# Kernel optimization log

Hardware: AMD Instinct MI355X
Metric: run time of the kernel (lower is better)

The kernel has to match this reference:

```python
import jax, jax.numpy as jnp
import numpy as np

C = 256          # channels
NUM_HEADS = 4
HEAD_DIM = C // NUM_HEADS
TILE_SIZE = 64
TILE_SEQ = TILE_SIZE * TILE_SIZE  # 4096
B, H_IMG, W_IMG = 1, 96, 96
EPS = 1e-5


def setup_inputs() -> dict:
    key = jax.random.key(0)
    k0, k1, k2 = jax.random.split(key, 3)
    x = jax.random.normal(k0, (B, C, H_IMG, W_IMG), jnp.float32)
    norm_w = jnp.ones((C,), jnp.float32)
    norm_b = jnp.zeros((C,), jnp.float32)
    qkv_w = jax.random.normal(k1, (3 * C, C), jnp.float32) * (C ** -0.5)
    qkv_b = jnp.zeros((3 * C,), jnp.float32)
    proj_w = jax.random.normal(k2, (C, C), jnp.float32) * (C ** -0.5)
    proj_b = jnp.zeros((C,), jnp.float32)
    return {"x": x, "norm_w": norm_w, "norm_b": norm_b,
            "qkv_w": qkv_w, "qkv_b": qkv_b,
            "proj_w": proj_w, "proj_b": proj_b}


def _attn(q, k, v, scale):
    # q: [B,H,Q,D], k/v: [B,H,K,D]
    s = jnp.einsum('bhqd,bhkd->bhqk', q, k) * scale
    p = jax.nn.softmax(s, axis=-1)
    return jnp.einsum('bhqk,bhkd->bhqd', p, v)


def reference(x, norm_w, norm_b, qkv_w, qkv_b, proj_w, proj_b):
    b, c, h, w = x.shape
    seq = h * w
    g = min(32, c)
    # GroupNorm
    xg = x.reshape(b, g, c // g, h, w)
    mean = xg.mean(axis=(2, 3, 4), keepdims=True)
    var = ((xg - mean) ** 2).mean(axis=(2, 3, 4), keepdims=True)
    xn = (xg - mean) * jax.lax.rsqrt(var + EPS)
    xn = xn.reshape(b, c, h, w) * norm_w[None, :, None, None] + norm_b[None, :, None, None]
    # flatten spatial -> tokens
    xf = xn.transpose(0, 2, 3, 1).reshape(b, seq, c)
    qkv = xf @ qkv_w.T + qkv_b  # [B,S,3C]
    qkv = qkv.reshape(b, seq, 3, NUM_HEADS, HEAD_DIM).transpose(2, 0, 3, 1, 4)
    q, k, v = qkv[0], qkv[1], qkv[2]  # [B,H,S,D]
    scale = HEAD_DIM ** -0.5
    if seq > TILE_SEQ:
        num_tiles = (seq + TILE_SEQ - 1) // TILE_SEQ
        outs = []
        for i in range(num_tiles):  # small fixed tile count, static slices
            s0 = i * TILE_SEQ
            e0 = min((i + 1) * TILE_SEQ, seq)
            k0 = max(0, s0 - TILE_SEQ // 2)
            k1 = min(seq, e0 + TILE_SEQ // 2)
            outs.append(_attn(q[:, :, s0:e0], k[:, :, k0:k1], v[:, :, k0:k1], scale))
        out = jnp.concatenate(outs, axis=2)
    else:
        out = _attn(q, k, v, scale)
    out = out.transpose(0, 2, 1, 3).reshape(b, seq, c)
    out = out @ proj_w.T + proj_b
    out = out.reshape(b, h, w, c).transpose(0, 3, 1, 2)
    return out + x
```

## Files before the change

### kernel.cpp

```cpp
#include <hip/hip_runtime.h>

typedef __bf16 bf16x8 __attribute__((ext_vector_type(8)));
typedef float f32x4 __attribute__((ext_vector_type(4)));
typedef float f32x16 __attribute__((ext_vector_type(16)));
typedef int i32x4 __attribute__((ext_vector_type(4)));
typedef int i32x2 __attribute__((ext_vector_type(2)));
typedef unsigned short u16x4 __attribute__((ext_vector_type(4)));

#define S_TOK 9216
#define LOG2E 1.44269504088896340736f
#define SCALE_Q (0.125f * LOG2E)

__device__ inline unsigned short f2bf(float f) {
    unsigned int u = __builtin_bit_cast(unsigned int, f);
    return (unsigned short)((u + 0x7fffu + ((u >> 16) & 1u)) >> 16);
}

__device__ inline unsigned int cvt_pk_bf16(float lo, float hi) {
    unsigned int r;
    asm("v_cvt_pk_bf16_f32 %0, %1, %2" : "=v"(r) : "v"(lo), "v"(hi));
    return r;
}

__device__ inline void permswap(unsigned int& a, unsigned int& b) {
    asm("v_permlane32_swap_b32 %0, %1" : "+v"(a), "+v"(b));
}

__device__ inline f32x4 MFMA(bf16x8 a, bf16x8 b, f32x4 c) {
    return __builtin_amdgcn_mfma_f32_16x16x32_bf16(a, b, c, 0, 0, 0);
}
__device__ inline f32x16 MFMA32(bf16x8 a, bf16x8 b, f32x16 c) {
    return __builtin_amdgcn_mfma_f32_32x32x16_bf16(a, b, c, 0, 0, 0);
}

__device__ inline int swz(int row, int c) {
    return ((c + (row >> 3)) & 7) ^ (row & 7);
}
__device__ inline bf16x8 load_frag(const unsigned short* lds, int outer, int kbase) {
    int lane = threadIdx.x & 63;
    int row = outer + (lane & 15);
    int cc = swz(row, (kbase >> 3) + (lane >> 4));
    return *reinterpret_cast<const bf16x8*>(lds + row * 64 + cc * 8);
}
__device__ inline bf16x8 load_frag32(const unsigned short* lds, int outer, int kbase) {
    int lane = threadIdx.x & 63;
    int row = outer + (lane & 31);
    int cc = swz(row, (kbase >> 3) + (lane >> 5));
    return *reinterpret_cast<const bf16x8*>(lds + row * 64 + cc * 8);
}
__device__ inline void stage_tile(unsigned short* lds, const unsigned short* src,
                                  int stride, int nrows) {
    for (int id = threadIdx.x; id < nrows * 8; id += 256) {
        int row = id >> 3, cc = id & 7;
        i32x4 v = *reinterpret_cast<const i32x4*>(src + row * stride + cc * 8);
        *reinterpret_cast<i32x4*>(lds + row * 64 + swz(row, cc) * 8) = v;
    }
}

__global__ __launch_bounds__(256) void gn_stats_part(const float* __restrict__ x,
                                                     float* __restrict__ part) {
    int c = blockIdx.x;
    const f32x4* p = reinterpret_cast<const f32x4*>(x + c * S_TOK);
    float s = 0.f, ss = 0.f;
    for (int i = threadIdx.x; i < 2304; i += 256) {
        f32x4 v = p[i];
        s += v[0] + v[1] + v[2] + v[3];
        ss += v[0] * v[0] + v[1] * v[1] + v[2] * v[2] + v[3] * v[3];
    }
#pragma unroll
    for (int off = 1; off < 64; off <<= 1) {
        s += __shfl_xor(s, off);
        ss += __shfl_xor(ss, off);
    }
    __shared__ float rs[4], rss[4];
    int wave = threadIdx.x >> 6;
    if ((threadIdx.x & 63) == 0) { rs[wave] = s; rss[wave] = ss; }
    __syncthreads();
    if (threadIdx.x == 0) {
        part[c] = rs[0] + rs[1] + rs[2] + rs[3];
        part[256 + c] = rss[0] + rss[1] + rss[2] + rss[3];
    }
}

__global__ __launch_bounds__(256) void gn_apply(const float* __restrict__ x,
                                                const float* __restrict__ part,
                                                const float* __restrict__ nw,
                                                const float* __restrict__ nb,
                                                unsigned short* __restrict__ xf) {
    __shared__ float tl[64][65];
    __shared__ float gmean[8], grstd[8];
    int sb = blockIdx.x * 64, cb = blockIdx.y * 64;
    if (threadIdx.x < 8) {
        int g = (cb >> 3) + threadIdx.x;
        float s = 0.f, ss = 0.f;
#pragma unroll
        for (int i = 0; i < 8; ++i) { s += part[g * 8 + i]; ss += part[256 + g * 8 + i]; }
        float mean = s * (1.f / 73728.f);
        float var = ss * (1.f / 73728.f) - mean * mean;
        gmean[threadIdx.x] = mean;
        grstd[threadIdx.x] = rsqrtf(var + 1e-5f);
    }
    __syncthreads();
    for (int id = threadIdx.x; id < 1024; id += 256) {
        int cr = id >> 4;
        int sq = (id & 15) << 2;
        int c = cb + cr;
        f32x4 v = *reinterpret_cast<const f32x4*>(x + c * S_TOK + sb + sq);
        float mu = gmean[cr >> 3], rstd = grstd[cr >> 3];
        float wv = nw[c] * rstd;
        float bv = nb[c] - mu * wv;
#pragma unroll
        for (int j = 0; j < 4; ++j) tl[sq + j][cr] = v[j] * wv + bv;
    }
    __syncthreads();
    for (int id = threadIdx.x; id < 1024; id += 256) {
        int sr = id >> 4;
        int cq = (id & 15) << 2;
        u16x4 o;
#pragma unroll
        for (int j = 0; j < 4; ++j) o[j] = f2bf(tl[sr][cq + j]);
        *reinterpret_cast<u16x4*>(xf + (sb + sr) * 256 + cb + cq) = o;
    }
}

__global__ __launch_bounds__(256) void conv_both(const float* __restrict__ qkvw_in,
                                                 const float* __restrict__ projw_in,
                                                 unsigned short* __restrict__ out) {
    int i = blockIdx.x * 256 + threadIdx.x;
    float v;
    if (i < 768 * 256) v = qkvw_in[i] * ((i < 256 * 256) ? SCALE_Q : 1.0f);
    else v = projw_in[i - 768 * 256];
    out[i] = f2bf(v);
}

template <int MODE>
__global__ __launch_bounds__(256) void gemm_bt(const unsigned short* __restrict__ A,
                                               const unsigned short* __restrict__ B,
                                               const float* __restrict__ bias,
                                               unsigned short* __restrict__ q_out,
                                               unsigned short* __restrict__ k_out,
                                               unsigned short* __restrict__ vT_out,
                                               const float* __restrict__ xres,
                                               float* __restrict__ out) {
    __shared__ alignas(16) unsigned short As[128 * 64];
    __shared__ alignas(16) unsigned short Bs[128 * 64];
    int mb = blockIdx.x, nb = blockIdx.y;
    int wave = threadIdx.x >> 6, lane = threadIdx.x & 63;
    int wm = wave >> 1, wn = wave & 1;
    f32x4 zero = {0.f, 0.f, 0.f, 0.f};
    f32x4 acc[4][4];
    for (int i = 0; i < 4; ++i)
        for (int j = 0; j < 4; ++j) acc[i][j] = zero;
    for (int ks = 0; ks < 4; ++ks) {
        __syncthreads();
        stage_tile(As, A + (mb * 128) * 256 + ks * 64, 256, 128);
        stage_tile(Bs, B + (nb * 128) * 256 + ks * 64, 256, 128);
        __syncthreads();
#pragma unroll
        for (int kk = 0; kk < 2; ++kk) {
            bf16x8 af[4], bfr[4];
#pragma unroll
            for (int mt = 0; mt < 4; ++mt) af[mt] = load_frag(As, wm * 64 + mt * 16, kk * 32);
#pragma unroll
            for (int nt = 0; nt < 4; ++nt) bfr[nt] = load_frag(Bs, wn * 64 + nt * 16, kk * 32);
#pragma unroll
            for (int mt = 0; mt < 4; ++mt)
#pragma unroll
                for (int nt = 0; nt < 4; ++nt)
                    acc[mt][nt] = MFMA(af[mt], bfr[nt], acc[mt][nt]);
        }
    }
    int r0 = (lane >> 4) << 2;
    int cl = lane & 15;
#pragma unroll
    for (int mt = 0; mt < 4; ++mt) {
#pragma unroll
        for (int nt = 0; nt < 4; ++nt) {
            int m = mb * 128 + wm * 64 + mt * 16 + r0;
            int n = nb * 128 + wn * 64 + nt * 16 + cl;
            if (MODE == 0) {
                float bv = bias[n] * ((n < 256) ? SCALE_Q : 1.0f);
                if (n < 256) {
#pragma unroll
                    for (int r = 0; r < 4; ++r)
                        q_out[(m + r) * 256 + n] = f2bf(acc[mt][nt][r] + bv);
                } else if (n < 512) {
#pragma unroll
                    for (int r = 0; r < 4; ++r)
                        k_out[(m + r) * 256 + (n - 256)] = f2bf(acc[mt][nt][r] + bv);
                } else {
                    u16x4 o;
#pragma unroll
                    for (int r = 0; r < 4; ++r) o[r] = f2bf(acc[mt][nt][r] + bv);
                    *reinterpret_cast<u16x4*>(vT_out + (n - 512) * S_TOK + m) = o;
                }
            } else {
                float bv = bias[n];
                f32x4 xr = *reinterpret_cast<const f32x4*>(xres + n * S_TOK + m);
                f32x4 o;
#pragma unroll
                for (int r = 0; r < 4; ++r) o[r] = acc[mt][nt][r] + bv + xr[r];
                *reinterpret_cast<f32x4*>(out + n * S_TOK + m) = o;
            }
        }
    }
}

struct StageRegs { i32x4 k0, k1, v0, v1; };

__device__ inline StageRegs load_stage(const unsigned short* ksrc, const unsigned short* vsrc) {
    int tid = threadIdx.x;
    int row = tid >> 3, cc = tid & 7;
    StageRegs r;
    r.k0 = *reinterpret_cast<const i32x4*>(ksrc + row * 256 + cc * 8);
    r.k1 = *reinterpret_cast<const i32x4*>(ksrc + (row + 32) * 256 + cc * 8);
    r.v0 = *reinterpret_cast<const i32x4*>(vsrc + row * S_TOK + cc * 8);
    r.v1 = *reinterpret_cast<const i32x4*>(vsrc + (row + 32) * S_TOK + cc * 8);
    return r;
}

__device__ inline void store_stage(unsigned short* K, unsigned short* V, StageRegs r) {
    int tid = threadIdx.x;
    int row = tid >> 3, cc = tid & 7;
    *reinterpret_cast<i32x4*>(K + row * 64 + swz(row, cc) * 8) = r.k0;
    *reinterpret_cast<i32x4*>(K + (row + 32) * 64 + swz(row + 32, cc) * 8) = r.k1;
    *reinterpret_cast<i32x4*>(V + row * 64 + swz(row, cc) * 8) = r.v0;
    *reinterpret_cast<i32x4*>(V + (row + 32) * 64 + swz(row + 32, cc) * 8) = r.v1;
}

__device__ inline bf16x8 mkpa(const f32x16& sc, int b, float& lrun) {
    float E0 = __builtin_amdgcn_exp2f(sc[b + 0]);
    float E1 = __builtin_amdgcn_exp2f(sc[b + 1]);
    float E2 = __builtin_amdgcn_exp2f(sc[b + 2]);
    float E3 = __builtin_amdgcn_exp2f(sc[b + 3]);
    float E4 = __builtin_amdgcn_exp2f(sc[b + 4]);
    float E5 = __builtin_amdgcn_exp2f(sc[b + 5]);
    float E6 = __builtin_amdgcn_exp2f(sc[b + 6]);
    float E7 = __builtin_amdgcn_exp2f(sc[b + 7]);
    lrun += ((E0 + E1) + (E2 + E3)) + ((E4 + E5) + (E6 + E7));
    unsigned int w0 = cvt_pk_bf16(E0, E1);
    unsigned int w1 = cvt_pk_bf16(E2, E3);
    unsigned int w2 = cvt_pk_bf16(E4, E5);
    unsigned int w3 = cvt_pk_bf16(E6, E7);
    permswap(w0, w2);
    permswap(w1, w3);
    i32x4 w;
    w[0] = (int)w0; w[1] = (int)w1; w[2] = (int)w2; w[3] = (int)w3;
    return __builtin_bit_cast(bf16x8, w);
}

template <int NC>
__global__ __launch_bounds__(256) void attn(const unsigned short* __restrict__ qb,
                                            const unsigned short* __restrict__ kb,
                                            const unsigned short* __restrict__ vT,
                                            unsigned short* __restrict__ Opart,
                                            float* __restrict__ lpart) {
    __shared__ alignas(16) unsigned short LDS[4 * 4096];
    unsigned short* Ks0 = LDS;
    unsigned short* Ks1 = LDS + 4096;
    unsigned short* Vs0 = LDS + 8192;
    unsigned short* Vs1 = LDS + 12288;
    constexpr int NS0 = 96 / NC, NS1 = 112 / NC, NS2 = 48 / NC;
    constexpr int B0 = 16 * NS0, B1 = B0 + 16 * NS1, NB = B1 + 4 * NS2;
    static_assert(NC % 2 == 0 && NC >= 4, "NC even");

    int bx = blockIdx.x;
    int head = bx / NB;
    int r = bx % NB;
    int tile, seg, qi;
    if (r < B0)      { tile = 0; seg = r >> 4; qi = r & 15; }
    else if (r < B1) { int t = r - B0; tile = 1; seg = t >> 4; qi = t & 15; }
    else             { int t = r - B1; tile = 2; seg = t >> 2; qi = t & 3; }
    int qs0 = (tile == 0) ? 0 : (tile == 1 ? 4096 : 8192);
    int kv0 = (tile == 0) ? 0 : (tile == 1 ? 2048 : 6144);
    int qstart = qs0 + qi * 256;
    int c0 = seg * NC;
    int wave = threadIdx.x >> 6, lane = threadIdx.x & 63;
    int l31 = lane & 31, h = lane >> 5;

    stage_tile(LDS, qb + qstart * 256 + head * 64, 256, 256);
    __syncthreads();
    bf16x8 qfA[4], qfB[4];
#pragma unroll
    for (int s = 0; s < 4; ++s) {
        qfA[s] = load_frag32(LDS, wave * 64, s * 16);
        qfB[s] = load_frag32(LDS, wave * 64 + 32, s * 16);
    }
    __syncthreads();

    f32x16 oA0, oA1, oB0, oB1;
#pragma unroll
    for (int i = 0; i < 16; ++i) { oA0[i] = 0.f; oA1[i] = 0.f; oB0[i] = 0.f; oB1[i] = 0.f; }
    float lA = 0.f, lB = 0.f;

    const unsigned short* kbase = kb + kv0 * 256 + head * 64;
    const unsigned short* vbase = vT + head * 64 * S_TOK + kv0;

    auto compute = [&](const unsigned short* Kp, const unsigned short* Vp) {
        __builtin_amdgcn_s_setprio(1);
#pragma unroll
        for (int half = 0; half < 2; ++half) {
            f32x16 sc0, sc1;
#pragma unroll
            for (int i = 0; i < 16; ++i) { sc0[i] = 0.f; sc1[i] = 0.f; }
#pragma unroll
            for (int s = 0; s < 4; ++s) {
                bf16x8 kf = load_frag32(Kp, half * 32, s * 16);
                sc0 = MFMA32(kf, qfA[s], sc0);
                sc1 = MFMA32(kf, qfB[s], sc1);
            }
#pragma unroll
            for (int sl = 0; sl < 2; ++sl) {
                bf16x8 paA = mkpa(sc0, 8 * sl, lA);
                bf16x8 paB = mkpa(sc1, 8 * sl, lB);
                int kvb = (half * 2 + sl) * 16;
                bf16x8 v0 = load_frag32(Vp, 0, kvb);
                bf16x8 v1 = load_frag32(Vp, 32, kvb);
                oA0 = MFMA32(paA, v0, oA0);
                oA1 = MFMA32(paA, v1, oA1);
                oB0 = MFMA32(paB, v0, oB0);
                oB1 = MFMA32(paB, v1, oB1);
            }
        }
        __builtin_amdgcn_s_setprio(0);
    };

    StageRegs Ra = load_stage(kbase + c0 * (64 * 256), vbase + c0 * 64);
    store_stage(Ks0, Vs0, Ra);
    Ra = load_stage(kbase + (c0 + 1) * (64 * 256), vbase + (c0 + 1) * 64);
    __syncthreads();

#pragma unroll
    for (int k = 0; k < NC; ++k) {
        const unsigned short* Kp = (k & 1) ? Ks1 : Ks0;
        const unsigned short* Vp = (k & 1) ? Vs1 : Vs0;
        if (k + 1 < NC) {
            store_stage((k & 1) ? Ks0 : Ks1, (k & 1) ? Vs0 : Vs1, Ra);
            if (k + 2 < NC)
                Ra = load_stage(kbase + (c0 + k + 2) * (64 * 256), vbase + (c0 + k + 2) * 64);
        }
        compute(Kp, Vp);
        __syncthreads();
    }

    unsigned int obase = (unsigned int)seg * (S_TOK * 256);
#pragma unroll
    for (int reg = 0; reg < 16; ++reg) {
        int qloc = (reg & 3) + 8 * (reg >> 2) + 4 * h;
        int sA = qstart + wave * 64 + qloc;
        int sB = sA + 32;
        Opart[obase + sA * 256 + head * 64 + l31] =
            __builtin_bit_cast(unsigned short, (__bf16)oA0[reg]);
        Opart[obase + sA * 256 + head * 64 + 32 + l31] =
            __builtin_bit_cast(unsigned short, (__bf16)oA1[reg]);
        Opart[obase + sB * 256 + head * 64 + l31] =
            __builtin_bit_cast(unsigned short, (__bf16)oB0[reg]);
        Opart[obase + sB * 256 + head * 64 + 32 + l31] =
            __builtin_bit_cast(unsigned short, (__bf16)oB1[reg]);
    }
    float lfA = lA + __shfl_xor(lA, 32);
    float lfB = lB + __shfl_xor(lB, 32);
    if (h == 0) {
        int sA = qstart + wave * 64 + l31;
        lpart[(seg * 4 + head) * S_TOK + sA] = lfA;
        lpart[(seg * 4 + head) * S_TOK + sA + 32] = lfB;
    }
}

template <int NC>
__global__ __launch_bounds__(256) void combine(const unsigned short* __restrict__ Op,
                                               const float* __restrict__ lp,
                                               unsigned short* __restrict__ att) {
    int idx = blockIdx.x * 256 + threadIdx.x;
    int s = idx >> 5;
    int c0 = (idx & 31) << 3;
    int head = c0 >> 6;
    int nseg = (s < 4096) ? (96 / NC) : (s < 8192 ? (112 / NC) : (48 / NC));
    float acc[8] = {0.f, 0.f, 0.f, 0.f, 0.f, 0.f, 0.f, 0.f};
    float l = 0.f;
    for (int seg = 0; seg < nseg; ++seg) {
        i32x4 v = *reinterpret_cast<const i32x4*>(Op + (size_t)seg * (S_TOK * 256) + s * 256 + c0);
        const unsigned short* u = reinterpret_cast<const unsigned short*>(&v);
#pragma unroll
        for (int i = 0; i < 8; ++i)
            acc[i] += __builtin_bit_cast(float, ((unsigned int)u[i]) << 16);
        l += lp[(seg * 4 + head) * S_TOK + s];
    }
    float inv = 1.f / l;
    u16x4 o0, o1;
#pragma unroll
    for (int i = 0; i < 4; ++i) {
        o0[i] = f2bf(acc[i] * inv);
        o1[i] = f2bf(acc[4 + i] * inv);
    }
    unsigned short* dst = att + s * 256 + c0;
    *reinterpret_cast<u16x4*>(dst) = o0;
    *reinterpret_cast<u16x4*>(dst + 4) = o1;
}

extern "C" void kernel_launch(void* const* d_in, const int* in_sizes, int n_in,
                              void* d_out, int out_size, void* d_ws, size_t ws_size,
                              hipStream_t stream) {
    const float* x      = (const float*)d_in[0];
    const float* norm_w = (const float*)d_in[1];
    const float* norm_b = (const float*)d_in[2];
    const float* qkv_w  = (const float*)d_in[3];
    const float* qkv_b  = (const float*)d_in[4];
    const float* proj_w = (const float*)d_in[5];
    const float* proj_b = (const float*)d_in[6];
    float* outp = (float*)d_out;

    char* wsb = (char*)d_ws;
    float* part = (float*)wsb;
    unsigned short* xf    = (unsigned short*)(wsb + 2048);
    unsigned short* qkvw  = xf + 9216 * 256;
    unsigned short* projw = qkvw + 768 * 256;
    unsigned short* qbuf  = projw + 256 * 256;
    unsigned short* kbuf  = qbuf + 9216 * 256;
    unsigned short* vTbuf = kbuf + 9216 * 256;
    unsigned short* Opart = vTbuf + 256 * 9216;
    size_t fixed_bytes = 2048 + 2ull * 256 * (9216ull * 4 + 768 + 256);
    size_t need8 = fixed_bytes + 2ull * 14 * 9216 * 256 + 4ull * 14 * 4 * 9216;
    bool use8 = (ws_size >= need8);
    int MS = use8 ? 14 : 7;
    float* lpart = (float*)(Opart + (size_t)MS * 9216 * 256);
    unsigned short* attb  = xf;

    gn_stats_part<<<dim3(256), dim3(256), 0, stream>>>(x, part);
    gn_apply<<<dim3(144, 4), dim3(256), 0, stream>>>(x, part, norm_w, norm_b, xf);
    conv_both<<<dim3(1024), dim3(256), 0, stream>>>(qkv_w, proj_w, qkvw);
    gemm_bt<0><<<dim3(72, 6), dim3(256), 0, stream>>>(xf, qkvw, qkv_b,
                                                      qbuf, kbuf, vTbuf, nullptr, nullptr);
    if (use8) {
        attn<8><<<dim3(4 * 440), dim3(256), 0, stream>>>(qbuf, kbuf, vTbuf, Opart, lpart);
        combine<8><<<dim3(1152), dim3(256), 0, stream>>>(Opart, lpart, attb);
    } else {
        attn<16><<<dim3(4 * 220), dim3(256), 0, stream>>>(qbuf, kbuf, vTbuf, Opart, lpart);
        combine<16><<<dim3(1152), dim3(256), 0, stream>>>(Opart, lpart, attb);
    }
    gemm_bt<1><<<dim3(72, 2), dim3(256), 0, stream>>>(attb, projw, proj_b,
                                                      nullptr, nullptr, nullptr, x, outp);
}
```

Before: 138.2 us.

## Replace split-K partial buffers and combine pass with float atomics fused into projection

The attention kernel now accumulates its un-normalized partial outputs and row sums directly into fp32 buffers with atomicAdd, replacing the per-segment bf16 partial buffers. The separate combine kernel is removed, and the projection GEMM applies the 1/l normalization and bf16 conversion while staging its A tile. This removes the large partial-buffer write/read traffic and one launch. In exchange it adds a zeroing kernel, fp32 atomic contention on the output rows, and non-deterministic summation order.

```diff
diff --git a/kernel.cpp b/kernel.cpp
--- a/kernel.cpp
+++ b/kernel.cpp
@@ -4,7 +4,6 @@
 typedef float f32x4 __attribute__((ext_vector_type(4)));
 typedef float f32x16 __attribute__((ext_vector_type(16)));
 typedef int i32x4 __attribute__((ext_vector_type(4)));
-typedef int i32x2 __attribute__((ext_vector_type(2)));
 typedef unsigned short u16x4 __attribute__((ext_vector_type(4)));
 
 #define S_TOK 9216
@@ -55,6 +54,12 @@
         i32x4 v = *reinterpret_cast<const i32x4*>(src + row * stride + cc * 8);
         *reinterpret_cast<i32x4*>(lds + row * 64 + swz(row, cc) * 8) = v;
     }
+}
+
+__global__ __launch_bounds__(256) void zero_f32(float* __restrict__ p, int n4) {
+    f32x4 z = {0.f, 0.f, 0.f, 0.f};
+    for (int i = blockIdx.x * 256 + threadIdx.x; i < n4; i += gridDim.x * 256)
+        reinterpret_cast<f32x4*>(p)[i] = z;
 }
 
 __global__ __launch_bounds__(256) void gn_stats_part(const float* __restrict__ x,
@@ -133,15 +138,12 @@
     out[i] = f2bf(v);
 }
 
-template <int MODE>
-__global__ __launch_bounds__(256) void gemm_bt(const unsigned short* __restrict__ A,
-                                               const unsigned short* __restrict__ B,
-                                               const float* __restrict__ bias,
-                                               unsigned short* __restrict__ q_out,
-                                               unsigned short* __restrict__ k_out,
-                                               unsigned short* __restrict__ vT_out,
-                                               const float* __restrict__ xres,
-                                               float* __restrict__ out) {
+__global__ __launch_bounds__(256) void gemm_qkv(const unsigned short* __restrict__ A,
+                                                const unsigned short* __restrict__ B,
+                                                const float* __restrict__ bias,
+                                                unsigned short* __restrict__ q_out,
+                                                unsigned short* __restrict__ k_out,
+                                                unsigned short* __restrict__ vT_out) {
     __shared__ alignas(16) unsigned short As[128 * 64];
     __shared__ alignas(16) unsigned short Bs[128 * 64];
     int mb = blockIdx.x, nb = blockIdx.y;
@@ -178,30 +180,86 @@
         for (int nt = 0; nt < 4; ++nt) {
             int m = mb * 128 + wm * 64 + mt * 16 + r0;
             int n = nb * 128 + wn * 64 + nt * 16 + cl;
-            if (MODE == 0) {
-                float bv = bias[n] * ((n < 256) ? SCALE_Q : 1.0f);
-                if (n < 256) {
-#pragma unroll
-                    for (int r = 0; r < 4; ++r)
-                        q_out[(m + r) * 256 + n] = f2bf(acc[mt][nt][r] + bv);
-                } else if (n < 512) {
-#pragma unroll
-                    for (int r = 0; r < 4; ++r)
-                        k_out[(m + r) * 256 + (n - 256)] = f2bf(acc[mt][nt][r] + bv);
-                } else {
-                    u16x4 o;
-#pragma unroll
-                    for (int r = 0; r < 4; ++r) o[r] = f2bf(acc[mt][nt][r] + bv);
-                    *reinterpret_cast<u16x4*>(vT_out + (n - 512) * S_TOK + m) = o;
-                }
+            float bv = bias[n] * ((n < 256) ? SCALE_Q : 1.0f);
+            if (n < 256) {
+#pragma unroll
+                for (int r = 0; r < 4; ++r)
+                    q_out[(m + r) * 256 + n] = f2bf(acc[mt][nt][r] + bv);
+            } else if (n < 512) {
+#pragma unroll
+                for (int r = 0; r < 4; ++r)
+                    k_out[(m + r) * 256 + (n - 256)] = f2bf(acc[mt][nt][r] + bv);
             } else {
-                float bv = bias[n];
-                f32x4 xr = *reinterpret_cast<const f32x4*>(xres + n * S_TOK + m);
-                f32x4 o;
-#pragma unroll
-                for (int r = 0; r < 4; ++r) o[r] = acc[mt][nt][r] + bv + xr[r];
-                *reinterpret_cast<f32x4*>(out + n * S_TOK + m) = o;
+                u16x4 o;
+#pragma unroll
+                for (int r = 0; r < 4; ++r) o[r] = f2bf(acc[mt][nt][r] + bv);
+                *reinterpret_cast<u16x4*>(vT_out + (n - 512) * S_TOK + m) = o;
             }
+        }
+    }
+}
+
+__global__ __launch_bounds__(256) void gemm_proj(const float* __restrict__ Of,
+                                                 const float* __restrict__ lsum,
+                                                 const unsigned short* __restrict__ Bw,
+                                                 const float* __restrict__ bias,
+                                                 const float* __restrict__ xres,
+                                                 float* __restrict__ out) {
+    __shared__ alignas(16) unsigned short As[128 * 64];
+    __shared__ alignas(16) unsigned short Bs[128 * 64];
+    int mb = blockIdx.x, nb = blockIdx.y;
+    int wave = threadIdx.x >> 6, lane = threadIdx.x & 63;
+    int wm = wave >> 1, wn = wave & 1;
+    f32x4 zero = {0.f, 0.f, 0.f, 0.f};
+    f32x4 acc[4][4];
+    for (int i = 0; i < 4; ++i)
+        for (int j = 0; j < 4; ++j) acc[i][j] = zero;
+    for (int ks = 0; ks < 4; ++ks) {
+        __syncthreads();
+        for (int id = threadIdx.x; id < 1024; id += 256) {
+            int row = id >> 3, cc = id & 7;
+            int s = mb * 128 + row;
+            const float* src = Of + s * 256 + ks * 64 + cc * 8;
+            f32x4 a = *reinterpret_cast<const f32x4*>(src);
+            f32x4 b = *reinterpret_cast<const f32x4*>(src + 4);
+            float inv = 1.f / lsum[ks * S_TOK + s];
+            i32x4 w;
+            w[0] = (int)cvt_pk_bf16(a[0] * inv, a[1] * inv);
+            w[1] = (int)cvt_pk_bf16(a[2] * inv, a[3] * inv);
+            w[2] = (int)cvt_pk_bf16(b[0] * inv, b[1] * inv);
+            w[3] = (int)cvt_pk_bf16(b[2] * inv, b[3] * inv);
+            *reinterpret_cast<i32x4*>(As + row * 64 + swz(row, cc) * 8) = w;
+        }
+        stage_tile(Bs, Bw + (nb * 128) * 256 + ks * 64, 256, 128);
+        __syncthreads();
+#pragma unroll
+        for (int kk = 0; kk < 2; ++kk) {
+            bf16x8 af[4], bfr[4];
+#pragma unroll
+            for (int mt = 0; mt < 4; ++mt) af[mt] = load_frag(As, wm * 64 + mt * 16, kk * 32);
+#pragma unroll
+            for (int nt = 0; nt < 4; ++nt) bfr[nt] = load_frag(Bs, wn * 64 + nt * 16, kk * 32);
+#pragma unroll
+            for (int mt = 0; mt < 4; ++mt)
+#pragma unroll
+                for (int nt = 0; nt < 4; ++nt)
+                    acc[mt][nt] = MFMA(af[mt], bfr[nt], acc[mt][nt]);
+        }
+    }
+    int r0 = (lane >> 4) << 2;
+    int cl = lane & 15;
+#pragma unroll
+    for (int mt = 0; mt < 4; ++mt) {
+#pragma unroll
+        for (int nt = 0; nt < 4; ++nt) {
+            int m = mb * 128 + wm * 64 + mt * 16 + r0;
+            int n = nb * 128 + wn * 64 + nt * 16 + cl;
+            float bv = bias[n];
+            f32x4 xr = *reinterpret_cast<const f32x4*>(xres + n * S_TOK + m);
+            f32x4 o;
+#pragma unroll
+            for (int r = 0; r < 4; ++r) o[r] = acc[mt][nt][r] + bv + xr[r];
+            *reinterpret_cast<f32x4*>(out + n * S_TOK + m) = o;
         }
     }
 }
@@ -253,8 +311,8 @@
 __global__ __launch_bounds__(256) void attn(const unsigned short* __restrict__ qb,
                                             const unsigned short* __restrict__ kb,
                                             const unsigned short* __restrict__ vT,
-                                            unsigned short* __restrict__ Opart,
-                                            float* __restrict__ lpart) {
+                                            float* __restrict__ Of,
+                                            float* __restrict__ lsum) {
     __shared__ alignas(16) unsigned short LDS[4 * 4096];
     unsigned short* Ks0 = LDS;
     unsigned short* Ks1 = LDS + 4096;
@@ -343,59 +401,23 @@
         __syncthreads();
     }
 
-    unsigned int obase = (unsigned int)seg * (S_TOK * 256);
 #pragma unroll
     for (int reg = 0; reg < 16; ++reg) {
         int qloc = (reg & 3) + 8 * (reg >> 2) + 4 * h;
         int sA = qstart + wave * 64 + qloc;
         int sB = sA + 32;
-        Opart[obase + sA * 256 + head * 64 + l31] =
-            __builtin_bit_cast(unsigned short, (__bf16)oA0[reg]);
-        Opart[obase + sA * 256 + head * 64 + 32 + l31] =
-            __builtin_bit_cast(unsigned short, (__bf16)oA1[reg]);
-        Opart[obase + sB * 256 + head * 64 + l31] =
-            __builtin_bit_cast(unsigned short, (__bf16)oB0[reg]);
-        Opart[obase + sB * 256 + head * 64 + 32 + l31] =
-            __builtin_bit_cast(unsigned short, (__bf16)oB1[reg]);
+        atomicAdd(&Of[sA * 256 + head * 64 + l31], oA0[reg]);
+        atomicAdd(&Of[sA * 256 + head * 64 + 32 + l31], oA1[reg]);
+        atomicAdd(&Of[sB * 256 + head * 64 + l31], oB0[reg]);
+        atomicAdd(&Of[sB * 256 + head * 64 + 32 + l31], oB1[reg]);
     }
     float lfA = lA + __shfl_xor(lA, 32);
     float lfB = lB + __shfl_xor(lB, 32);
     if (h == 0) {
         int sA = qstart + wave * 64 + l31;
-        lpart[(seg * 4 + head) * S_TOK + sA] = lfA;
-        lpart[(seg * 4 + head) * S_TOK + sA + 32] = lfB;
-    }
-}
-
-template <int NC>
-__global__ __launch_bounds__(256) void combine(const unsigned short* __restrict__ Op,
-                                               const float* __restrict__ lp,
-                                               unsigned short* __restrict__ att) {
-    int idx = blockIdx.x * 256 + threadIdx.x;
-    int s = idx >> 5;
-    int c0 = (idx & 31) << 3;
-    int head = c0 >> 6;
-    int nseg = (s < 4096) ? (96 / NC) : (s < 8192 ? (112 / NC) : (48 / NC));
-    float acc[8] = {0.f, 0.f, 0.f, 0.f, 0.f, 0.f, 0.f, 0.f};
-    float l = 0.f;
-    for (int seg = 0; seg < nseg; ++seg) {
-        i32x4 v = *reinterpret_cast<const i32x4*>(Op + (size_t)seg * (S_TOK * 256) + s * 256 + c0);
-        const unsigned short* u = reinterpret_cast<const unsigned short*>(&v);
-#pragma unroll
-        for (int i = 0; i < 8; ++i)
-            acc[i] += __builtin_bit_cast(float, ((unsigned int)u[i]) << 16);
-        l += lp[(seg * 4 + head) * S_TOK + s];
-    }
-    float inv = 1.f / l;
-    u16x4 o0, o1;
-#pragma unroll
-    for (int i = 0; i < 4; ++i) {
-        o0[i] = f2bf(acc[i] * inv);
-        o1[i] = f2bf(acc[4 + i] * inv);
-    }
-    unsigned short* dst = att + s * 256 + c0;
-    *reinterpret_cast<u16x4*>(dst) = o0;
-    *reinterpret_cast<u16x4*>(dst + 4) = o1;
+        atomicAdd(&lsum[head * S_TOK + sA], lfA);
+        atomicAdd(&lsum[head * S_TOK + sA + 32], lfB);
+    }
 }
 
 extern "C" void kernel_launch(void* const* d_in, const int* in_sizes, int n_in,
@@ -418,26 +440,15 @@
     unsigned short* qbuf  = projw + 256 * 256;
     unsigned short* kbuf  = qbuf + 9216 * 256;
     unsigned short* vTbuf = kbuf + 9216 * 256;
-    unsigned short* Opart = vTbuf + 256 * 9216;
-    size_t fixed_bytes = 2048 + 2ull * 256 * (9216ull * 4 + 768 + 256);
-    size_t need8 = fixed_bytes + 2ull * 14 * 9216 * 256 + 4ull * 14 * 4 * 9216;
-    bool use8 = (ws_size >= need8);
-    int MS = use8 ? 14 : 7;
-    float* lpart = (float*)(Opart + (size_t)MS * 9216 * 256);
-    unsigned short* attb  = xf;
-
+    float* Of   = (float*)(vTbuf + 256 * 9216);
+    float* lsum = Of + 9216 * 256;
+
+    int n4 = (9216 * 256 + 4 * S_TOK) / 4;
+    zero_f32<<<dim3(1024), dim3(256), 0, stream>>>(Of, n4);
     gn_stats_part<<<dim3(256), dim3(256), 0, stream>>>(x, part);
     gn_apply<<<dim3(144, 4), dim3(256), 0, stream>>>(x, part, norm_w, norm_b, xf);
     conv_both<<<dim3(1024), dim3(256), 0, stream>>>(qkv_w, proj_w, qkvw);
-    gemm_bt<0><<<dim3(72, 6), dim3(256), 0, stream>>>(xf, qkvw, qkv_b,
-                                                      qbuf, kbuf, vTbuf, nullptr, nullptr);
-    if (use8) {
-        attn<8><<<dim3(4 * 440), dim3(256), 0, stream>>>(qbuf, kbuf, vTbuf, Opart, lpart);
-        combine<8><<<dim3(1152), dim3(256), 0, stream>>>(Opart, lpart, attb);
-    } else {
-        attn<16><<<dim3(4 * 220), dim3(256), 0, stream>>>(qbuf, kbuf, vTbuf, Opart, lpart);
-        combine<16><<<dim3(1152), dim3(256), 0, stream>>>(Opart, lpart, attb);
-    }
-    gemm_bt<1><<<dim3(72, 2), dim3(256), 0, stream>>>(attb, projw, proj_b,
-                                                      nullptr, nullptr, nullptr, x, outp);
-}
+    gemm_qkv<<<dim3(72, 6), dim3(256), 0, stream>>>(xf, qkvw, qkv_b, qbuf, kbuf, vTbuf);
+    attn<8><<<dim3(4 * 440), dim3(256), 0, stream>>>(qbuf, kbuf, vTbuf, Of, lsum);
+    gemm_proj<<<dim3(72, 2), dim3(256), 0, stream>>>(Of, lsum, projw, proj_b, x, outp);
+}
```

Result: slower. 175.4 us (+26.9%).
